# Kernel optimization log

Measured on AMD Instinct MI355X. Metric: run time of the kernel, lower is better.

## Reference

```python
import jax, jax.numpy as jnp
import numpy as np

B, U, I, H = 4096, 6, 1024, 512
IK, IV, K = 64, 400, 4
CH, CK, CV = 4, 32, 512
NS = 4


def setup_inputs() -> dict:
    key = jax.random.key(0)
    ks = jax.random.split(key, 14)
    s = 0.02
    return dict(
        x=jax.random.normal(ks[0], (B, 1, I), jnp.float32),
        hs=jax.random.normal(ks[1], (B, U, H), jnp.float32),
        Wk=jax.random.normal(ks[2], (I, IK), jnp.float32) * s,
        bk=jnp.zeros((IK,), jnp.float32),
        Wv=jax.random.normal(ks[3], (I, IV), jnp.float32) * s,
        bv=jnp.zeros((IV,), jnp.float32),
        Wq=jax.random.normal(ks[4], (U, H, IK), jnp.float32) * s,
        Wq_=jax.random.normal(ks[5], (U, H, CH * CK), jnp.float32) * s,
        Wk_=jax.random.normal(ks[6], (U, H, CH * CK), jnp.float32) * s,
        Wv_=jax.random.normal(ks[7], (U, H, CH * CV), jnp.float32) * s,
        Wo_=jax.random.normal(ks[8], (U, CH * CV, CV), jnp.float32) * s,
        sw=jax.nn.softmax(jax.random.normal(ks[9], (U, NS), jnp.float32), axis=-1),
        gru_wx=jax.random.normal(ks[10], (NS, IV, 3 * H), jnp.float32) * s,
        gru_wh=jax.random.normal(ks[11], (NS, H, 3 * H), jnp.float32) * s,
    )


def reference(x, hs, Wk, bk, Wv, bv, Wq, Wq_, Wk_, Wv_, Wo_, sw, gru_wx, gru_wh):
    b = x.shape[0]
    # append null input along token dim -> (B, 2, I)
    x2 = jnp.concatenate([x, jnp.zeros_like(x)], axis=1)
    # input attention (num_input_heads = 1)
    k_l = x2 @ Wk + bk                                   # (B,2,IK)
    v_l = x2 @ Wv + bv                                   # (B,2,IV)
    q_l = jnp.einsum('buh,uhd->bud', hs, Wq)             # (B,U,IK)
    scores = jnp.einsum('bud,btd->but', q_l, k_l) / np.sqrt(IK).astype(np.float32)
    # top-k gating on the non-null score
    not_null = scores[:, :, 0]                           # (B,U)
    _, idx = jax.lax.top_k(not_null, K)
    mask = jnp.zeros((b, U), x.dtype).at[jnp.arange(b)[:, None], idx].set(1.0)
    probs = jax.nn.softmax(scores, axis=-1)              # dropout off (eval)
    inputs = jnp.einsum('but,btv->buv', probs, v_l) * mask[:, :, None]  # (B,U,IV)
    # shared-schema GroupGRU: per-unit weights = schema mixture
    Wx = jnp.einsum('us,sio->uio', sw, gru_wx)           # (U,IV,3H)
    Wh = jnp.einsum('us,sho->uho', sw, gru_wh)           # (U,H,3H)
    gx = jnp.einsum('bui,uio->buo', inputs, Wx)
    gh = jnp.einsum('buh,uho->buo', hs, Wh)
    xr, xz, xn = jnp.split(gx, 3, axis=-1)
    hr, hz, hn = jnp.split(gh, 3, axis=-1)
    r = jax.nn.sigmoid(xr + hr)
    z = jax.nn.sigmoid(xz + hz)
    n = jnp.tanh(xn + r * hn)
    hy = n + z * (hs - n)                                # (B,U,H)
    # blocked_grad is identity in forward
    h_b = hy
    # communication attention (4 heads)
    q = jnp.einsum('buh,uho->buo', h_b, Wq_).reshape(b, U, CH, CK).transpose(0, 2, 1, 3)
    kk = jnp.einsum('buh,uho->buo', h_b, Wk_).reshape(b, U, CH, CK).transpose(0, 2, 1, 3)
    v = jnp.einsum('buh,uho->buo', h_b, Wv_).reshape(b, U, CH, CV).transpose(0, 2, 1, 3)
    att = jnp.einsum('bhqd,bhkd->bhqk', q, kk) / np.sqrt(CK).astype(np.float32)
    ap = jax.nn.softmax(att, axis=-1) * mask[:, None, :, None]  # mask query units
    ctx = jnp.einsum('bhqk,bhkd->bhqd', ap, v)           # (B,CH,U,CV)
    ctx = ctx.transpose(0, 2, 1, 3).reshape(b, U, CH * CV)
    ctx = jnp.einsum('buh,uho->buo', ctx, Wo_) + h_b     # (B,U,H)
    m = mask[:, :, None]
    hs_new = m * ctx + (1.0 - m) * hs
    return hs_new
```

## Files before the change

### kernel.cpp

```cpp
#include <hip/hip_runtime.h>
#include <cstddef>
#include <cstdint>


typedef unsigned short u16;
typedef __bf16 bf16x8 __attribute__((ext_vector_type(8)));
typedef float f32x4 __attribute__((ext_vector_type(4)));
typedef u16 u16x4 __attribute__((ext_vector_type(4)));

#define DEVFN static __device__ __forceinline__

DEVFN float ldin(const void* p, size_t i, int f) {
  return f ? (float)reinterpret_cast<const __bf16*>(p)[i]
           : reinterpret_cast<const float*>(p)[i];
}
DEVFN float bf2f(const u16* p, size_t i) {
  return (float)reinterpret_cast<const __bf16*>(p)[i];
}
DEVFN void f2bf(u16* p, size_t i, float v) {
  reinterpret_cast<__bf16*>(p)[i] = (__bf16)v;
}
DEVFN u16 bfbits(float v) {
  __bf16 b = (__bf16)v;
  return *reinterpret_cast<u16*>(&b);
}
DEVFN void gload16(const __bf16* g, __bf16* l) {
  __builtin_amdgcn_global_load_lds(
      (const __attribute__((address_space(1))) void*)g,
      (__attribute__((address_space(3))) void*)l, 16, 0, 0);
}

constexpr size_t OFF_FLAG = 0;
constexpr size_t OFF_MASK = 256;
constexpr size_t OFF_WVT  = 98560;
constexpr size_t OFF_WQKV = 1147136;
constexpr size_t OFF_WOT  = 15302912;
constexpr size_t OFF_WXCT = 27885824;
constexpr size_t OFF_WHCT = 35553536;
constexpr size_t OFF_HY   = 44990720;
constexpr size_t OFF_XB   = 70156544;
constexpr size_t OFF_HSB  = 78545152;
constexpr size_t ARENA    = 103710976;
constexpr size_t A_INP    = ARENA;
constexpr size_t A_PK     = ARENA;
constexpr size_t A_PQ     = ARENA + 4194304;
constexpr size_t A_P1     = 124158208;
constexpr size_t A_KL     = A_P1;
constexpr size_t A_QL     = A_P1 + 1048576;
constexpr size_t A_VL     = A_P1 + 7340032;

__global__ void rim_detect(const void* sw, int* flagp) {
  if (threadIdx.x == 0) {
    float s = 0.f;
    for (int i = 0; i < 24; i++)
      s += (float)reinterpret_cast<const __bf16*>(sw)[i];
    flagp[0] = (s > 5.5f && s < 6.5f) ? 1 : 0;
  }
}

__global__ __launch_bounds__(256)
void rim_cast(const void* __restrict__ in, u16* __restrict__ out, long n8,
              const int* __restrict__ flagp)
{
  const int f = flagp[0];
  long stride = (long)gridDim.x * 256;
  for (long u = (long)blockIdx.x * 256 + threadIdx.x; u < n8; u += stride) {
    if (f) {
      reinterpret_cast<uint4*>(out)[u] = reinterpret_cast<const uint4*>(in)[u];
    } else {
      f32x4 lo = reinterpret_cast<const f32x4*>(in)[u * 2];
      f32x4 hi = reinterpret_cast<const f32x4*>(in)[u * 2 + 1];
      bf16x8 r;
#pragma unroll
      for (int q = 0; q < 4; q++) { r[q] = (__bf16)lo[q]; r[q + 4] = (__bf16)hi[q]; }
      reinterpret_cast<bf16x8*>(out)[u] = r;
    }
  }
}

__global__ __launch_bounds__(256)
void rim_sgemm32(const void* __restrict__ A_, long lda, long Az,
                 const void* __restrict__ W_, long Wz,
                 float* __restrict__ P, int KC,
                 const int* __restrict__ flagp)
{
  const int f = flagp[0];
  __shared__ float As[32 * 33];
  __shared__ float Ws[32 * 68];
  const int t = threadIdx.x;
  const int m0 = blockIdx.x * 32, kc = blockIdx.y, z = blockIdx.z;
  const int Z = gridDim.z;
  const int kb = kc * KC;
  const int tx = t & 15, ty = t >> 4;

  f32x4 acc[2];
#pragma unroll
  for (int i = 0; i < 2; i++)
#pragma unroll
    for (int j = 0; j < 4; j++) acc[i][j] = 0.f;

  for (int k0 = kb; k0 < kb + KC; k0 += 32) {
#pragma unroll
    for (int j = 0; j < 4; j++) {
      int idx = t + j * 256;
      int row = idx >> 5, kk = idx & 31;
      As[row * 33 + kk] =
          ldin(A_, (size_t)(m0 + row) * lda + (size_t)z * Az + k0 + kk, f);
    }
#pragma unroll
    for (int j = 0; j < 8; j++) {
      int idx = t + j * 256;
      int kk = idx >> 6, n = idx & 63;
      Ws[kk * 68 + n] = ldin(W_, (size_t)z * Wz + (size_t)(k0 + kk) * 64 + n, f);
    }
    __syncthreads();
#pragma unroll 8
    for (int kk = 0; kk < 32; kk++) {
      f32x4 wv = *reinterpret_cast<const f32x4*>(&Ws[kk * 68 + tx * 4]);
#pragma unroll
      for (int i = 0; i < 2; i++) {
        float a = As[(ty * 2 + i) * 33 + kk];
#pragma unroll
        for (int j = 0; j < 4; j++) acc[i][j] += a * wv[j];
      }
    }
    __syncthreads();
  }
  float* Pb = P + ((size_t)kc * Z + z) * (4096 * 64);
#pragma unroll
  for (int i = 0; i < 2; i++)
    *reinterpret_cast<f32x4*>(&Pb[(size_t)(m0 + ty * 2 + i) * 64 + tx * 4]) = acc[i];
}

__global__ void rim_sreduce(const float* __restrict__ P, int NK, int Z,
                            float* __restrict__ C, long ldc, long Cz,
                            const void* __restrict__ bias,
                            const int* __restrict__ flagp, long total)
{
  const int f = flagp[0];
  long idx = (long)blockIdx.x * 256 + threadIdx.x;
  if (idx >= total) return;
  long z = idx / (4096 * 64);
  long r = idx - z * (4096 * 64);
  long m = r >> 6;
  int n = (int)(r & 63);
  float s = bias ? ldin(bias, n, f) : 0.f;
  for (int kc = 0; kc < NK; kc++)
    s += P[((size_t)kc * Z + z) * (4096 * 64) + r];
  C[(size_t)m * ldc + (size_t)z * Cz + n] = s;
}

template<int EPI>
__global__ __launch_bounds__(256)
void rim_gemm(const u16* __restrict__ A16, long A0, long lda, long Az,
              const u16* __restrict__ B_, long Bz,
              void* __restrict__ C_, long C0, long ldc, long Cz,
              int M, int N, int K,
              const void* __restrict__ bias,
              const u16* __restrict__ hyp,
              const float* __restrict__ maskp,
              const void* __restrict__ hsp,
              const int* __restrict__ flagp)
{
  __shared__ __align__(16) __bf16 As[2][128 * 32];
  __shared__ __align__(16) __bf16 Bs[2][128 * 32];
  const int f = flagp[0];
  const int t = threadIdx.x;

  int gx = gridDim.x, gy = gridDim.y;
  int nwg = gx * gy * (int)gridDim.z;
  int wg = blockIdx.x + gx * (blockIdx.y + gy * blockIdx.z);
  {
    int q = nwg >> 3, r = nwg & 7, xc = wg & 7, ix = wg >> 3;
    wg = (xc < r ? xc * (q + 1) : r * (q + 1) + (xc - r) * q) + ix;
  }
  const int mb = wg % gx;
  const int nb = (wg / gx) % gy;
  const int z  = wg / (gx * gy);
  const int m0 = mb * 128, n0 = nb * 128;

  const __bf16* Ab = reinterpret_cast<const __bf16*>(A16) + (size_t)A0 +
                     (size_t)z * Az + (size_t)m0 * lda;
  const __bf16* Bb = reinterpret_cast<const __bf16*>(B_) + (size_t)z * Bz +
                     (size_t)n0 * (size_t)K;

  const int lane = t & 63, w = t >> 6;
  const int srow = lane >> 2;
  const int skq  = (lane & 3) * 8;
  const __bf16* aS0 = Ab + (size_t)(w * 16 + srow) * lda + skq;
  const __bf16* aS1 = Ab + (size_t)((w + 4) * 16 + srow) * lda + skq;
  const __bf16* bS0 = Bb + (size_t)(w * 16 + srow) * (size_t)K + skq;
  const __bf16* bS1 = Bb + (size_t)((w + 4) * 16 + srow) * (size_t)K + skq;

  const int wm = (w & 1) * 64, wn = (w >> 1) * 64;
  const int lr = lane & 15, lk = (lane >> 4) * 8;

  f32x4 acc[4][4];
#pragma unroll
  for (int i = 0; i < 4; i++)
#pragma unroll
    for (int j = 0; j < 4; j++)
#pragma unroll
      for (int r = 0; r < 4; r++) acc[i][j][r] = 0.f;

  auto STAGE = [&](int buf, int k0) {
    gload16(aS0 + k0, &As[buf][w * 512]);
    gload16(aS1 + k0, &As[buf][(w + 4) * 512]);
    gload16(bS0 + k0, &Bs[buf][w * 512]);
    gload16(bS1 + k0, &Bs[buf][(w + 4) * 512]);
  };

  STAGE(0, 0);
  int cur = 0;
  for (int k0 = 0; k0 < K; k0 += 32) {
    __syncthreads();
    if (k0 + 32 < K) STAGE(cur ^ 1, k0 + 32);
    bf16x8 af[4], bg[4];
#pragma unroll
    for (int i = 0; i < 4; i++)
      af[i] = *reinterpret_cast<const bf16x8*>(&As[cur][(wm + i * 16 + lr) * 32 + lk]);
#pragma unroll
    for (int j = 0; j < 4; j++)
      bg[j] = *reinterpret_cast<const bf16x8*>(&Bs[cur][(wn + j * 16 + lr) * 32 + lk]);
#pragma unroll
    for (int i = 0; i < 4; i++)
#pragma unroll
      for (int j = 0; j < 4; j++)
        acc[i][j] = __builtin_amdgcn_mfma_f32_16x16x32_bf16(af[i], bg[j], acc[i][j], 0, 0, 0);
    cur ^= 1;
  }

  const int rq = (lane >> 4) * 4;
  const int cq = lane & 15;
#pragma unroll
  for (int i = 0; i < 4; i++) {
#pragma unroll
    for (int j = 0; j < 4; j++) {
      int cg = n0 + wn + j * 16 + cq;
      if (cg >= N) continue;
#pragma unroll
      for (int r = 0; r < 4; r++) {
        int rg = m0 + wm + i * 16 + rq + r;
        if (rg >= M) continue;
        float v = acc[i][j][r];
        size_t cidx = (size_t)rg * ldc + (size_t)z * Cz + cg;
        if constexpr (EPI == 2) {
          f2bf((u16*)C_, C0 + cidx, v + ldin(bias, cg, f));
        } else if constexpr (EPI == 3) {
          f2bf((u16*)C_, C0 + cidx, v);
        } else {
          float mk = maskp[(size_t)rg * 6 + z];
          if (mk > 0.5f) {
            float o = v + bf2f(hyp, cidx);
            if (f) f2bf((u16*)C_, C0 + cidx, o);
            else   reinterpret_cast<float*>(C_)[C0 + cidx] = o;
          } else {
            if (f) reinterpret_cast<u16*>(C_)[C0 + cidx] =
                       reinterpret_cast<const u16*>(hsp)[C0 + cidx];
            else   reinterpret_cast<float*>(C_)[C0 + cidx] =
                       reinterpret_cast<const float*>(hsp)[C0 + cidx];
          }
        }
      }
    }
  }
}

__global__ __launch_bounds__(256)
void rim_gemm_pair(const u16* __restrict__ A1, long A01, long lda1, long Az1,
                   const u16* __restrict__ B1, long Bz1,
                   u16* __restrict__ C1, int K1,
                   const u16* __restrict__ A2, long A02, long lda2, long Az2,
                   const u16* __restrict__ B2, long Bz2,
                   u16* __restrict__ C2, int K2,
                   long ldc, long Cz, int M, int N)
{
  __shared__ __align__(16) __bf16 As[2][128 * 32];
  __shared__ __align__(16) __bf16 Bs[2][128 * 32];
  const int t = threadIdx.x;

  int gx = gridDim.x, gy = gridDim.y;
  int nwg = gx * gy * (int)gridDim.z;
  int wg = blockIdx.x + gx * (blockIdx.y + gy * blockIdx.z);
  {
    int q = nwg >> 3, r = nwg & 7, xc = wg & 7, ix = wg >> 3;
    wg = (xc < r ? xc * (q + 1) : r * (q + 1) + (xc - r) * q) + ix;
  }
  const int mb = wg % gx;
  const int nb = (wg / gx) % gy;
  const int zz = wg / (gx * gy);
  const int m0 = mb * 128, n0 = nb * 128;

  const int sel = (zz < 6) ? 0 : 1;
  const int z   = sel ? zz - 6 : zz;
  const int K   = sel ? K2 : K1;
  const __bf16* Ab = sel
      ? reinterpret_cast<const __bf16*>(A2) + (size_t)A02 + (size_t)z * Az2 +
        (size_t)m0 * lda2
      : reinterpret_cast<const __bf16*>(A1) + (size_t)A01 + (size_t)z * Az1 +
        (size_t)m0 * lda1;
  const long lda = sel ? lda2 : lda1;
  const __bf16* Bb = sel
      ? reinterpret_cast<const __bf16*>(B2) + (size_t)z * Bz2 + (size_t)n0 * K
      : reinterpret_cast<const __bf16*>(B1) + (size_t)z * Bz1 + (size_t)n0 * K;
  u16* Cp = sel ? C2 : C1;

  const int lane = t & 63, w = t >> 6;
  const int srow = lane >> 2;
  const int skq  = (lane & 3) * 8;
  const __bf16* aS0 = Ab + (size_t)(w * 16 + srow) * lda + skq;
  const __bf16* aS1 = Ab + (size_t)((w + 4) * 16 + srow) * lda + skq;
  const __bf16* bS0 = Bb + (size_t)(w * 16 + srow) * (size_t)K + skq;
  const __bf16* bS1 = Bb + (size_t)((w + 4) * 16 + srow) * (size_t)K + skq;

  const int wm = (w & 1) * 64, wn = (w >> 1) * 64;
  const int lr = lane & 15, lk = (lane >> 4) * 8;

  f32x4 acc[4][4];
#pragma unroll
  for (int i = 0; i < 4; i++)
#pragma unroll
    for (int j = 0; j < 4; j++)
#pragma unroll
      for (int r = 0; r < 4; r++) acc[i][j][r] = 0.f;

  auto STAGE = [&](int buf, int k0) {
    gload16(aS0 + k0, &As[buf][w * 512]);
    gload16(aS1 + k0, &As[buf][(w + 4) * 512]);
    gload16(bS0 + k0, &Bs[buf][w * 512]);
    gload16(bS1 + k0, &Bs[buf][(w + 4) * 512]);
  };

  STAGE(0, 0);
  int cur = 0;
  for (int k0 = 0; k0 < K; k0 += 32) {
    __syncthreads();
    if (k0 + 32 < K) STAGE(cur ^ 1, k0 + 32);
    bf16x8 af[4], bg[4];
#pragma unroll
    for (int i = 0; i < 4; i++)
      af[i] = *reinterpret_cast<const bf16x8*>(&As[cur][(wm + i * 16 + lr) * 32 + lk]);
#pragma unroll
    for (int j = 0; j < 4; j++)
      bg[j] = *reinterpret_cast<const bf16x8*>(&Bs[cur][(wn + j * 16 + lr) * 32 + lk]);
#pragma unroll
    for (int i = 0; i < 4; i++)
#pragma unroll
      for (int j = 0; j < 4; j++)
        acc[i][j] = __builtin_amdgcn_mfma_f32_16x16x32_bf16(af[i], bg[j], acc[i][j], 0, 0, 0);
    cur ^= 1;
  }

  const int rq = (lane >> 4) * 4;
  const int cq = lane & 15;
#pragma unroll
  for (int i = 0; i < 4; i++) {
#pragma unroll
    for (int j = 0; j < 4; j++) {
      int cg = n0 + wn + j * 16 + cq;
      if (cg >= N) continue;
#pragma unroll
      for (int r = 0; r < 4; r++) {
        int rg = m0 + wm + i * 16 + rq + r;
        if (rg >= M) continue;
        f2bf(Cp, (size_t)rg * ldc + (size_t)z * Cz + cg, acc[i][j][r]);
      }
    }
  }
}

__global__ __launch_bounds__(256)
void rim_transpose(const void* __restrict__ in, u16* __restrict__ out,
                   int N, int Np, int K, long in_z, long out_z,
                   const int* __restrict__ flagp)
{
  const int f = flagp[0];
  __shared__ float tile[32][33];
  int z = blockIdx.z;
  int k0 = blockIdx.x * 32, n0 = blockIdx.y * 32;
  int c = threadIdx.x & 31, r = threadIdx.x >> 5;
  for (int rr = r; rr < 32; rr += 8) {
    int k = k0 + rr, n = n0 + c;
    tile[rr][c] = (k < K && n < N)
        ? ldin(in, (size_t)z * in_z + (size_t)k * N + n, f) : 0.f;
  }
  __syncthreads();
  for (int rr = r; rr < 32; rr += 8) {
    int n = n0 + rr, k = k0 + c;
    if (n < Np && k < K)
      f2bf(out, (size_t)z * out_z + (size_t)n * K + k, tile[c][rr]);
  }
}

__global__ __launch_bounds__(256)
void rim_gruw(const void* __restrict__ sw, const void* __restrict__ gw,
              u16* __restrict__ out, int IVp, int IVs,
              const int* __restrict__ flagp)
{
  const int f = flagp[0];
  __shared__ float lds[64 * 17];
  int u = blockIdx.z;
  int i0 = blockIdx.x * 16, o0 = blockIdx.y * 64;
  int t = threadIdx.x;
  float s0 = ldin(sw, u * 4 + 0, f), s1 = ldin(sw, u * 4 + 1, f);
  float s2 = ldin(sw, u * 4 + 2, f), s3 = ldin(sw, u * 4 + 3, f);
  int oo = t & 63, iq = t >> 6;
  size_t pl = (size_t)IVs * 1536;
#pragma unroll
  for (int r = 0; r < 4; r++) {
    int ii = iq * 4 + r;
    float acc = 0.f;
    if (i0 + ii < IVs) {
      size_t base = (size_t)(i0 + ii) * 1536 + o0 + oo;
      acc = s0 * ldin(gw, base, f) + s1 * ldin(gw, pl + base, f) +
            s2 * ldin(gw, 2 * pl + base, f) + s3 * ldin(gw, 3 * pl + base, f);
    }
    lds[oo * 17 + ii] = acc;
  }
  __syncthreads();
  int ow = t >> 2, iw = (t & 3) * 4;
  u16x4 pk;
#pragma unroll
  for (int j = 0; j < 4; j++) pk[j] = bfbits(lds[ow * 17 + iw + j]);
  *reinterpret_cast<u16x4*>(out + ((size_t)u * 1536 + o0 + ow) * IVp + i0 + iw) = pk;
}

__global__ __launch_bounds__(256)
void rim_scores(const float* __restrict__ q_l, const float* __restrict__ k_l0,
                const void* __restrict__ bk, const u16* __restrict__ v_l0,
                const void* __restrict__ bv, float* __restrict__ maskf,
                u16* __restrict__ inputs, const int* __restrict__ flagp)
{
  const int f = flagp[0];
  int b = blockIdx.x;
  int t = threadIdx.x;
  int lane = t & 63;
  __shared__ float s0[6], s1[6], sm[6], sp[6];
  if (t < 64) {
    float kv = k_l0[(size_t)b * 64 + lane];
    for (int u = 0; u < 6; u++) {
      float p = q_l[((size_t)b * 6 + u) * 64 + lane] * kv;
      for (int off = 32; off; off >>= 1) p += __shfl_down(p, off);
      if (lane == 0) s0[u] = p * 0.125f;
    }
  } else if (t < 128) {
    float kv = ldin(bk, lane, f);
    for (int u = 0; u < 6; u++) {
      float p = q_l[((size_t)b * 6 + u) * 64 + lane] * kv;
      for (int off = 32; off; off >>= 1) p += __shfl_down(p, off);
      if (lane == 0) s1[u] = p * 0.125f;
    }
  }
  __syncthreads();
  if (t == 0) {
    for (int u = 0; u < 6; u++) {
      int cnt = 0;
      for (int u2 = 0; u2 < 6; u2++)
        if (s0[u2] > s0[u] || (s0[u2] == s0[u] && u2 < u)) cnt++;
      float mk = (cnt < 4) ? 1.0f : 0.0f;
      sm[u] = mk;
      maskf[(size_t)b * 6 + u] = mk;
      sp[u] = 1.0f / (1.0f + expf(s1[u] - s0[u]));
    }
  }
  __syncthreads();
  for (int idx = t; idx < 2496; idx += 256) {
    int u = idx / 416, j = idx - u * 416;
    float val = 0.f;
    if (j < 400)
      val = sm[u] * (sp[u] * bf2f(v_l0, (size_t)b * 400 + j) +
                     (1.0f - sp[u]) * ldin(bv, j, f));
    f2bf(inputs, ((size_t)b * 6 + u) * 416 + j, val);
  }
}

__global__ __launch_bounds__(256)
void rim_gru(const u16* __restrict__ Ggx, const u16* __restrict__ Ggh,
             const void* __restrict__ hs, long R0,
             u16* __restrict__ hy, long total8,
             const int* __restrict__ flagp)
{
  const int f = flagp[0];
  long i8 = (long)blockIdx.x * 256 + threadIdx.x;
  if (i8 >= total8) return;
  long bu = i8 >> 6;
  int h0 = (int)(i8 & 63) * 8;
  size_t gb = ((size_t)bu * 1536 + h0) >> 3;
  const bf16x8* gx8 = reinterpret_cast<const bf16x8*>(Ggx);
  const bf16x8* gh8 = reinterpret_cast<const bf16x8*>(Ggh);
  bf16x8 xr8 = gx8[gb], xz8 = gx8[gb + 64], xn8 = gx8[gb + 128];
  bf16x8 hr8 = gh8[gb], hz8 = gh8[gb + 64], hn8 = gh8[gb + 128];
  float hv[8];
  size_t base = (size_t)R0 + (size_t)i8 * 8;
  if (f) {
    bf16x8 h8 = *reinterpret_cast<const bf16x8*>(
        reinterpret_cast<const __bf16*>(hs) + base);
#pragma unroll
    for (int j = 0; j < 8; j++) hv[j] = (float)h8[j];
  } else {
    f32x4 lo = *reinterpret_cast<const f32x4*>(
        reinterpret_cast<const float*>(hs) + base);
    f32x4 hi = *reinterpret_cast<const f32x4*>(
        reinterpret_cast<const float*>(hs) + base + 4);
#pragma unroll
    for (int j = 0; j < 4; j++) { hv[j] = lo[j]; hv[j + 4] = hi[j]; }
  }
  bf16x8 out;
#pragma unroll
  for (int j = 0; j < 8; j++) {
    float xr = (float)xr8[j], xz = (float)xz8[j], xn = (float)xn8[j];
    float hr = (float)hr8[j], hz = (float)hz8[j], hn = (float)hn8[j];
    float r = 1.f / (1.f + expf(-(xr + hr)));
    float zz = 1.f / (1.f + expf(-(xz + hz)));
    float n = tanhf(xn + r * hn);
    out[j] = (__bf16)(n + zz * (hv[j] - n));
  }
  *reinterpret_cast<bf16x8*>(hy + i8 * 8) = out;
}

__global__ __launch_bounds__(256)
void rim_attn(const u16* __restrict__ comb, const float* __restrict__ maskp,
              u16* __restrict__ ctx)
{
  int bl = blockIdx.x;
  int t = threadIdx.x;
  const __bf16* cb = reinterpret_cast<const __bf16*>(comb) + (size_t)bl * 13824;
  __shared__ float qs[1536];
  __shared__ float aps[144];
  __shared__ __align__(16) u16 vs[12288];
  if (t < 192) {
    int u = t >> 5, r8 = t & 31;
    bf16x8 q8 = *reinterpret_cast<const bf16x8*>(cb + u * 2304 + r8 * 8);
#pragma unroll
    for (int j = 0; j < 8; j++) qs[u * 256 + r8 * 8 + j] = (float)q8[j];
  }
  for (int idx = t; idx < 1536; idx += 256) {
    int u = idx >> 8, r = idx & 255;
    *reinterpret_cast<bf16x8*>(&vs[idx * 8]) =
        *reinterpret_cast<const bf16x8*>(cb + u * 2304 + 256 + r * 8);
  }
  __syncthreads();
  if (t < 144) {
    int h = t / 36, r6 = t % 36, uq = r6 / 6, uk = r6 % 6;
    float s = 0.f;
#pragma unroll
    for (int d = 0; d < 32; d++)
      s += qs[uq * 256 + h * 32 + d] * qs[uk * 256 + 128 + h * 32 + d];
    aps[t] = s * 0.17677669529663687f;
  }
  __syncthreads();
  if (t < 24) {
    int h = t / 6, uq = t % 6;
    float* row = &aps[h * 36 + uq * 6];
    float mx = row[0];
    for (int k = 1; k < 6; k++) mx = fmaxf(mx, row[k]);
    float e[6], sum = 0.f;
    for (int k = 0; k < 6; k++) { e[k] = expf(row[k] - mx); sum += e[k]; }
    float mk = maskp[(size_t)bl * 6 + uq] / sum;
    for (int k = 0; k < 6; k++) row[k] = e[k] * mk;
  }
  __syncthreads();
  for (int g8 = t; g8 < 1536; g8 += 256) {
    int uq = g8 >> 8;
    int g0 = (g8 & 255) * 8;
    int h  = g0 >> 9;
    const float* ar = &aps[h * 36 + uq * 6];
    float acc[8];
#pragma unroll
    for (int j = 0; j < 8; j++) acc[j] = 0.f;
#pragma unroll
    for (int k = 0; k < 6; k++) {
      bf16x8 vv = *reinterpret_cast<const bf16x8*>(&vs[k * 2048 + g0]);
      float a = ar[k];
#pragma unroll
      for (int j = 0; j < 8; j++) acc[j] += a * (float)vv[j];
    }
    bf16x8 ov;
#pragma unroll
    for (int j = 0; j < 8; j++) ov[j] = (__bf16)acc[j];
    *reinterpret_cast<bf16x8*>(
        &ctx[(((size_t)bl * 6 + uq) * 2048 + g0)]) = ov;
  }
}

extern "C" void kernel_launch(void* const* d_in, const int* in_sizes, int n_in,
                              void* d_out, int out_size, void* d_ws, size_t ws_size,
                              hipStream_t stream)
{
  (void)in_sizes; (void)n_in; (void)out_size;
  const void* x   = d_in[0];
  const void* hs  = d_in[1];
  const void* Wk  = d_in[2];
  const void* bk  = d_in[3];
  const void* Wv  = d_in[4];
  const void* bv  = d_in[5];
  const void* Wq  = d_in[6];
  const void* Wq_ = d_in[7];
  const void* Wk_ = d_in[8];
  const void* Wv_ = d_in[9];
  const void* Wo_ = d_in[10];
  const void* sw  = d_in[11];
  const void* gwx = d_in[12];
  const void* gwh = d_in[13];
  char* ws = (char*)d_ws;

  int*   flagp = (int*)(ws + OFF_FLAG);
  float* maskf = (float*)(ws + OFF_MASK);
  u16* WvT   = (u16*)(ws + OFF_WVT);
  u16* WQKV  = (u16*)(ws + OFF_WQKV);
  u16* WoT   = (u16*)(ws + OFF_WOT);
  u16* WxcT  = (u16*)(ws + OFF_WXCT);
  u16* WhcT  = (u16*)(ws + OFF_WHCT);
  u16* hy    = (u16*)(ws + OFF_HY);
  u16* xb    = (u16*)(ws + OFF_XB);
  u16* hsb   = (u16*)(ws + OFF_HSB);
  u16* inputs = (u16*)(ws + A_INP);
  float* PK   = (float*)(ws + A_PK);
  float* PQ   = (float*)(ws + A_PQ);
  float* k_l0 = (float*)(ws + A_KL);
  float* q_l  = (float*)(ws + A_QL);
  u16* v_l0   = (u16*)(ws + A_VL);

  int R2 = 256, R3 = 256;
  {
    const int cand[5] = {4096, 2048, 1024, 512, 256};
    for (int i = 0; i < 5; i++)
      if (A_P1 + (size_t)cand[i] * 36864 <= ws_size) { R2 = cand[i]; break; }
    for (int i = 0; i < 5; i++)
      if (ARENA + (size_t)cand[i] * 52224 <= ws_size) { R3 = cand[i]; break; }
  }

  rim_detect<<<dim3(1), dim3(64), 0, stream>>>(sw, flagp);

  rim_cast<<<dim3(2048), dim3(256), 0, stream>>>(x, xb, 524288L, flagp);
  rim_cast<<<dim3(2048), dim3(256), 0, stream>>>(hs, hsb, 1572864L, flagp);

  auto T = [&](const void* in, u16* outp, int N, int Np, int K, long iz, long oz,
               int Z) {
    dim3 g((K + 31) / 32, (Np + 31) / 32, Z);
    rim_transpose<<<g, dim3(256), 0, stream>>>(in, outp, N, Np, K, iz, oz, flagp);
  };
  T(Wv, WvT, 400, 512, 1024, 0, 0, 1);
  T(Wq_, WQKV, 128, 128, 512, 65536, 1179648, 6);
  T(Wk_, WQKV + 65536, 128, 128, 512, 65536, 1179648, 6);
  T(Wv_, WQKV + 131072, 2048, 2048, 512, 1048576, 1179648, 6);
  T(Wo_, WoT, 512, 512, 2048, 1048576, 1048576, 6);
  rim_gruw<<<dim3(26, 24, 6), dim3(256), 0, stream>>>(sw, gwx, WxcT, 416, 400, flagp);
  rim_gruw<<<dim3(32, 24, 6), dim3(256), 0, stream>>>(sw, gwh, WhcT, 512, 512, flagp);

  auto G = [&](int epi, const void* A, long A0, long lda, long Az,
               const u16* B, long Bz, void* C, long C0, long ldc, long Cz,
               int M, int N, int K, int Z,
               const void* bias, const u16* hyp, const float* mp, const void* hsp) {
    dim3 g((M + 127) / 128, (N + 127) / 128, Z), blk(256);
    if (epi == 2)
      rim_gemm<2><<<g, blk, 0, stream>>>((const u16*)A, A0, lda, Az, B, Bz, C, C0,
                                         ldc, Cz, M, N, K, bias, hyp, mp, hsp, flagp);
    else if (epi == 3)
      rim_gemm<3><<<g, blk, 0, stream>>>((const u16*)A, A0, lda, Az, B, Bz, C, C0,
                                         ldc, Cz, M, N, K, bias, hyp, mp, hsp, flagp);
    else
      rim_gemm<4><<<g, blk, 0, stream>>>((const u16*)A, A0, lda, Az, B, Bz, C, C0,
                                         ldc, Cz, M, N, K, bias, hyp, mp, hsp, flagp);
  };

  rim_sgemm32<<<dim3(128, 4, 1), dim3(256), 0, stream>>>(
      x, 1024, 0, Wk, 0, PK, 256, flagp);
  rim_sgemm32<<<dim3(128, 2, 6), dim3(256), 0, stream>>>(
      hs, 3072, 512, Wq, 32768, PQ, 256, flagp);
  rim_sreduce<<<dim3(1024), dim3(256), 0, stream>>>(
      PK, 4, 1, k_l0, 64, 0, bk, flagp, 4096L * 64);
  rim_sreduce<<<dim3(6144), dim3(256), 0, stream>>>(
      PQ, 2, 6, q_l, 384, 64, nullptr, flagp, 6L * 4096 * 64);
  G(2, xb, 0, 1024, 0, WvT, 0, v_l0, 0, 400, 0, 4096, 400, 1024, 1,
    bv, nullptr, nullptr, nullptr);
  rim_scores<<<dim3(4096), dim3(256), 0, stream>>>(q_l, k_l0, bk, v_l0, bv,
                                                   maskf, inputs, flagp);

  u16* Ggx = (u16*)(ws + A_P1);
  u16* Ggh = (u16*)(ws + A_P1 + (size_t)R2 * 18432);
  for (int r0 = 0; r0 < 4096; r0 += R2) {
    dim3 g(R2 / 128, 12, 12), blk(256);
    rim_gemm_pair<<<g, blk, 0, stream>>>(
        hsb, (long)r0 * 3072, 3072, 512, WhcT, 786432, Ggh, 512,
        inputs, (long)r0 * 2496, 2496, 416, WxcT, 638976, Ggx, 416,
        9216, 1536, R2, 1536);
    long total8 = (long)R2 * 3072 / 8;
    rim_gru<<<dim3((unsigned)(total8 / 256)), dim3(256), 0, stream>>>(
        Ggx, Ggh, hs, (long)r0 * 3072, hy + (size_t)r0 * 3072, total8, flagp);
  }

  u16* comb  = (u16*)(ws + ARENA);
  u16* ctx_c = (u16*)(ws + ARENA + (size_t)R3 * 27648);
  for (int r0 = 0; r0 < 4096; r0 += R3) {
    G(3, hy, (long)r0 * 3072, 3072, 512, WQKV, 1179648, comb, 0, 13824, 2304,
      R3, 2304, 512, 6, nullptr, nullptr, nullptr, nullptr);
    rim_attn<<<dim3(R3), dim3(256), 0, stream>>>(comb, maskf + (size_t)r0 * 6, ctx_c);
    G(4, ctx_c, 0, 12288, 2048, WoT, 1048576, d_out, (long)r0 * 3072, 3072, 512,
      R3, 512, 2048, 6, nullptr, hy + (size_t)r0 * 3072, maskf + (size_t)r0 * 6, hs);
  }
}
```

Measured before the change: 922.6 us.

## Triple-buffer LDS tiles with explicit vmcnt waits in GEMM kernels

Both MFMA GEMM kernels move from a double-buffered to a triple-buffered LDS pipeline that prefetches two K-tiles ahead. The __syncthreads is replaced by a partial s_waitcnt vmcnt(4) plus s_barrier, so only the oldest tile's global loads must land before compute and more memory latency can overlap with MFMA work. LDS use grows by half (48KB per block), which may lower occupancy. Correctness depends on the hand-counted vmcnt matching the four loads issued per stage and on the compiler not reordering around the sched barriers.

Result: no change. 931.2 us (+0.9%).

```diff
diff --git a/kernel.cpp b/kernel.cpp
--- a/kernel.cpp
+++ b/kernel.cpp
@@ -162,8 +162,8 @@
               const void* __restrict__ hsp,
               const int* __restrict__ flagp)
 {
-  __shared__ __align__(16) __bf16 As[2][128 * 32];
-  __shared__ __align__(16) __bf16 Bs[2][128 * 32];
+  __shared__ __align__(16) __bf16 As[3][128 * 32];
+  __shared__ __align__(16) __bf16 Bs[3][128 * 32];
   const int f = flagp[0];
   const int t = threadIdx.x;
 
@@ -210,11 +210,18 @@
     gload16(bS1 + k0, &Bs[buf][(w + 4) * 512]);
   };
 
+  const int NT = K >> 5;
   STAGE(0, 0);
+  if (NT > 1) STAGE(1, 32);
+  if (NT > 1) asm volatile("s_waitcnt vmcnt(4)" ::: "memory");
+  else        asm volatile("s_waitcnt vmcnt(0)" ::: "memory");
+  __builtin_amdgcn_s_barrier();
+  __builtin_amdgcn_sched_barrier(0);
+
   int cur = 0;
-  for (int k0 = 0; k0 < K; k0 += 32) {
-    __syncthreads();
-    if (k0 + 32 < K) STAGE(cur ^ 1, k0 + 32);
+  for (int s = 0; s < NT; ++s) {
+    const bool st2 = (s + 2 < NT);
+    if (st2) STAGE((cur + 2) % 3, (s + 2) * 32);
     bf16x8 af[4], bg[4];
 #pragma unroll
     for (int i = 0; i < 4; i++)
@@ -227,7 +234,14 @@
 #pragma unroll
       for (int j = 0; j < 4; j++)
         acc[i][j] = __builtin_amdgcn_mfma_f32_16x16x32_bf16(af[i], bg[j], acc[i][j], 0, 0, 0);
-    cur ^= 1;
+    if (s + 1 < NT) {
+      __builtin_amdgcn_sched_barrier(0);
+      if (st2) asm volatile("s_waitcnt vmcnt(4)" ::: "memory");
+      else     asm volatile("s_waitcnt vmcnt(0)" ::: "memory");
+      __builtin_amdgcn_s_barrier();
+      __builtin_amdgcn_sched_barrier(0);
+    }
+    cur = (cur + 1) % 3;
   }
 
   const int rq = (lane >> 4) * 4;
@@ -275,8 +289,8 @@
                    u16* __restrict__ C2, int K2,
                    long ldc, long Cz, int M, int N)
 {
-  __shared__ __align__(16) __bf16 As[2][128 * 32];
-  __shared__ __align__(16) __bf16 Bs[2][128 * 32];
+  __shared__ __align__(16) __bf16 As[3][128 * 32];
+  __shared__ __align__(16) __bf16 Bs[3][128 * 32];
   const int t = threadIdx.x;
 
   int gx = gridDim.x, gy = gridDim.y;
@@ -331,11 +345,18 @@
     gload16(bS1 + k0, &Bs[buf][(w + 4) * 512]);
   };
 
+  const int NT = K >> 5;
   STAGE(0, 0);
+  if (NT > 1) STAGE(1, 32);
+  if (NT > 1) asm volatile("s_waitcnt vmcnt(4)" ::: "memory");
+  else        asm volatile("s_waitcnt vmcnt(0)" ::: "memory");
+  __builtin_amdgcn_s_barrier();
+  __builtin_amdgcn_sched_barrier(0);
+
   int cur = 0;
-  for (int k0 = 0; k0 < K; k0 += 32) {
-    __syncthreads();
-    if (k0 + 32 < K) STAGE(cur ^ 1, k0 + 32);
+  for (int s = 0; s < NT; ++s) {
+    const bool st2 = (s + 2 < NT);
+    if (st2) STAGE((cur + 2) % 3, (s + 2) * 32);
     bf16x8 af[4], bg[4];
 #pragma unroll
     for (int i = 0; i < 4; i++)
@@ -348,7 +369,14 @@
 #pragma unroll
       for (int j = 0; j < 4; j++)
         acc[i][j] = __builtin_amdgcn_mfma_f32_16x16x32_bf16(af[i], bg[j], acc[i][j], 0, 0, 0);
-    cur ^= 1;
+    if (s + 1 < NT) {
+      __builtin_amdgcn_sched_barrier(0);
+      if (st2) asm volatile("s_waitcnt vmcnt(4)" ::: "memory");
+      else     asm volatile("s_waitcnt vmcnt(0)" ::: "memory");
+      __builtin_amdgcn_s_barrier();
+      __builtin_amdgcn_sched_barrier(0);
+    }
+    cur = (cur + 1) % 3;
   }
 
   const int rq = (lane >> 4) * 4;
```
